# Kernel optimization log

Hardware: AMD Instinct MI355X
Metric: run time of the kernel (lower is better)

The kernel has to match this reference:

```python
import jax, jax.numpy as jnp
import numpy as np

# Module config (matches init_kwargs)
H, W = 512, 512          # in_dims
KH, KW = 32, 32          # kernel_dims
SH, SW = 16, 16          # stride
PH, PW = 8, 8            # padding
B = 64                   # batch
FULL_H, FULL_W = H + 2 * PH, W + 2 * PW            # 528, 528
NKH = 1 + (FULL_H - KH) // SH                      # 32
NKW = 1 + (FULL_W - KW) // SW                      # 32
NK = NKH * NKW                                     # 1024 output positions


def _patch_indices() -> np.ndarray:
    """Flat indices into the padded image for each sliding window.

    Reproduces the connectivity matrix columns of _create_connectivity_matrix:
    window k starts at (row*SH)*FULL_W + col*SW. Returns (NK, KH*KW) int32.
    """
    dr, dc = np.meshgrid(np.arange(KH), np.arange(KW), indexing="ij")
    off = (dr * FULL_W + dc).reshape(-1)                       # (KH*KW,)
    starts = (np.arange(NKH)[:, None] * SH * FULL_W
              + np.arange(NKW)[None, :] * SW).reshape(-1)      # (NK,)
    return (starts[:, None] + off[None, :]).astype(np.int32)


_IDX = jnp.asarray(_patch_indices())  # (NK, KH*KW), constant layout


def setup_inputs() -> dict:
    key = jax.random.key(0)
    kx, kw, kb = jax.random.split(key, 3)
    x = jax.random.normal(kx, (B, 1, H, W), dtype=jnp.float32)
    # Per-window weights = BSR values of the masked dense (padded_total, NK) matrix.
    # Xavier-normal scale of the underlying dense linear.
    std = float(np.sqrt(2.0 / (FULL_H * FULL_W + NK)))
    weight = jax.random.normal(kw, (NK, KH * KW), dtype=jnp.float32) * std
    bias = jax.random.normal(kb, (NK,), dtype=jnp.float32) * 0.01
    return {"x": x, "weight": weight, "bias": bias}


def reference(x, weight, bias):
    # x: (B, 1, H, W) -> pad -> flatten to (B, FULL_H*FULL_W)
    xp = jnp.pad(x, ((0, 0), (0, 0), (PH, PH), (PW, PW)))
    xf = xp.reshape(x.shape[0], FULL_H * FULL_W)
    # Gather the KHxKW window for every output position: (B, NK, KH*KW).
    patches = jnp.take(xf, _IDX, axis=1)
    # Untied locally-connected contraction (the block-sparse GEMM) + bias.
    out = jnp.einsum("bnk,nk->bn", patches, weight) + bias
    return out.reshape(x.shape[0], NKH, NKW)
```

## Files before the change

### kernel.cpp

```cpp
#include <hip/hip_runtime.h>

#define IMG_H 512
#define IMG_W 512
#define IMG_SZ (IMG_H * IMG_W)
#define NKH 32
#define NKW 32
#define NK 1024
#define BATCH 64
#define NTT 33
#define NTILE (NTT * NTT)
#define BG 4
#define NBLK (NTILE * BG)

typedef __attribute__((address_space(3))) char lds_char_t;
typedef const __attribute__((address_space(1))) char g_char_t;

__global__ __launch_bounds__(256)
void bslc_init(const float* __restrict__ bias, float* __restrict__ out)
{
    const int g = blockIdx.x * 256 + threadIdx.x;
    out[g] = bias[g & (NK - 1)];
}

__global__ __launch_bounds__(256, 8)
void bslc_main(const float* __restrict__ x,
               const float* __restrict__ w,
               float* __restrict__ out)
{
    __shared__ float4 xs[16 * 64];

    const int hw = blockIdx.x;
    const int xcd = hw & 7, sl = hw >> 3;
    const int q8 = NBLK >> 3, r8 = NBLK & 7;
    const int work = (xcd < r8 ? xcd * (q8 + 1)
                               : r8 * (q8 + 1) + (xcd - r8) * q8) + sl;

    const int bg  = work & 3;
    const int lin = work >> 2;
    const int tr = lin / NTT, tc = lin % NTT;

    const int t = threadIdx.x, lane = t & 63, wv = t >> 6;

    const int r0 = tr * 16 - 8, c0 = tc * 16 - 8;
    const bool interior = (tr >= 1) & (tr <= 31) & (tc >= 1) & (tc <= 31);

    if (interior) {
#pragma unroll
        for (int ii = 0; ii < 4; ++ii) {
            const int bl = 4 * ii + wv;
            const int c  = lane ^ bl;
            const int rimg = r0 + (c >> 2);
            const int cimg = c0 + (c & 3) * 4;
            const float* gp = x + (size_t)(bg * 16 + bl) * IMG_SZ
                            + (size_t)rimg * IMG_W + cimg;
            __builtin_amdgcn_global_load_lds(
                (g_char_t*)gp, (lds_char_t*)&xs[bl * 64], 16, 0, 0);
        }
    } else {
#pragma unroll
        for (int ii = 0; ii < 4; ++ii) {
            const int bl = 4 * ii + wv;
            const int c  = lane ^ bl;
            const int rimg = r0 + (c >> 2);
            const int cimg = c0 + (c & 3) * 4;
            float4 v = make_float4(0.f, 0.f, 0.f, 0.f);
            if (rimg >= 0 && rimg < IMG_H && cimg >= 0 && cimg < IMG_W)
                v = *reinterpret_cast<const float4*>(
                    x + (size_t)(bg * 16 + bl) * IMG_SZ
                      + (size_t)rimg * IMG_W + cimg);
            xs[bl * 64 + lane] = v;
        }
    }
    __syncthreads();

    const int qr = wv >> 1, qc = wv & 1;
    const int nr = tr - qr, nc = tc - qc;
    if (nr < 0 || nr >= NKH || nc < 0 || nc >= NKW) return;
    const int n = nr * NKW + nc;

    const int p  = lane >> 4;
    const int bl = lane & 15;
    const float* wq = w + (size_t)n * 1024 + (size_t)(qr * 16) * 32 + qc * 16;

    float a0 = 0.f, a1 = 0.f, a2 = 0.f, a3 = 0.f;
#pragma unroll
    for (int j = 0; j < 16; ++j) {
        const int kq = p * 16 + j;
        const float4 xv  = xs[bl * 64 + (kq ^ bl)];
        const float4 wv4 = *reinterpret_cast<const float4*>(
            wq + (kq >> 2) * 32 + (kq & 3) * 4);
        a0 = fmaf(xv.x, wv4.x, a0);
        a1 = fmaf(xv.y, wv4.y, a1);
        a2 = fmaf(xv.z, wv4.z, a2);
        a3 = fmaf(xv.w, wv4.w, a3);
    }
    float s = (a0 + a1) + (a2 + a3);
    s += __shfl_xor(s, 16, 64);
    s += __shfl_xor(s, 32, 64);
    if (p == 0)
        atomicAdd(&out[(size_t)(bg * 16 + bl) * NK + n], s);
}

extern "C" void kernel_launch(void* const* d_in, const int* in_sizes, int n_in,
                              void* d_out, int out_size, void* d_ws, size_t ws_size,
                              hipStream_t stream) {
    const float* x    = (const float*)d_in[0];
    const float* wgt  = (const float*)d_in[1];
    const float* bias = (const float*)d_in[2];
    float* out        = (float*)d_out;

    bslc_init<<<dim3(BATCH * NK / 256), 256, 0, stream>>>(bias, out);
    bslc_main<<<dim3(NBLK), 256, 0, stream>>>(x, wgt, out);
}
```

Baseline: 112.5 us.

## Restructure locally-connected kernel into per-image-row waves with register-resident weights

Each wave now owns one image row and eight batch images. It keeps the weight slices for the two overlapping output rows in registers and streams row segments straight from global memory. This removes the LDS tile staging and barrier, and the weights are reused across eight images instead of being reloaded per tile. In exchange, lanes combine partial sums with cross-lane shuffles, and the kernel issues many more atomicAdds per output, since every image row contributes its own partial sum, raising atomic contention on the output.

```diff
diff --git a/kernel.cpp b/kernel.cpp
--- a/kernel.cpp
+++ b/kernel.cpp
@@ -3,17 +3,9 @@
 #define IMG_H 512
 #define IMG_W 512
 #define IMG_SZ (IMG_H * IMG_W)
-#define NKH 32
-#define NKW 32
 #define NK 1024
-#define BATCH 64
-#define NTT 33
-#define NTILE (NTT * NTT)
-#define BG 4
-#define NBLK (NTILE * BG)
-
-typedef __attribute__((address_space(3))) char lds_char_t;
-typedef const __attribute__((address_space(1))) char g_char_t;
+#define NWAVE 4096
+#define NBLK (NWAVE / 4)
 
 __global__ __launch_bounds__(256)
 void bslc_init(const float* __restrict__ bias, float* __restrict__ out)
@@ -22,83 +14,103 @@
     out[g] = bias[g & (NK - 1)];
 }
 
-__global__ __launch_bounds__(256, 8)
+__global__ __launch_bounds__(256)
 void bslc_main(const float* __restrict__ x,
                const float* __restrict__ w,
                float* __restrict__ out)
 {
-    __shared__ float4 xs[16 * 64];
+    const int bid  = blockIdx.x;
+    const int work = (bid & 7) * (NBLK / 8) + (bid >> 3);
+    const int gw   = work * 4 + (threadIdx.x >> 6);
+    const int lane = threadIdx.x & 63;
 
-    const int hw = blockIdx.x;
-    const int xcd = hw & 7, sl = hw >> 3;
-    const int q8 = NBLK >> 3, r8 = NBLK & 7;
-    const int work = (xcd < r8 ? xcd * (q8 + 1)
-                               : r8 * (q8 + 1) + (xcd - r8) * q8) + sl;
+    const int r  = gw >> 3;
+    const int b0 = (gw & 7) * 8;
 
-    const int bg  = work & 3;
-    const int lin = work >> 2;
-    const int tr = lin / NTT, tc = lin % NTT;
+    const int cpr = r + 8;
+    const int nrh = cpr >> 4, krh = cpr & 15;
+    const int nrl = nrh - 1,  krl = krh + 16;
+    const bool vh = (nrh < 32);
+    const bool vl = (nrl >= 0);
 
-    const int t = threadIdx.x, lane = t & 63, wv = t >> 6;
+    const int  m    = (lane + 1) >> 1;
+    const int  kc0  = (lane & 1) ? 0 : 8;
+    const bool vhc  = (m < 32);
+    const bool vlc  = (m >= 1);
 
-    const int r0 = tr * 16 - 8, c0 = tc * 16 - 8;
-    const bool interior = (tr >= 1) & (tr <= 31) & (tc >= 1) & (tc <= 31);
+    const float4 z4 = make_float4(0.f, 0.f, 0.f, 0.f);
+    float4 whh[2] = {z4, z4}, whl[2] = {z4, z4};
+    float4 wlh[2] = {z4, z4}, wll[2] = {z4, z4};
 
-    if (interior) {
-#pragma unroll
-        for (int ii = 0; ii < 4; ++ii) {
-            const int bl = 4 * ii + wv;
-            const int c  = lane ^ bl;
-            const int rimg = r0 + (c >> 2);
-            const int cimg = c0 + (c & 3) * 4;
-            const float* gp = x + (size_t)(bg * 16 + bl) * IMG_SZ
-                            + (size_t)rimg * IMG_W + cimg;
-            __builtin_amdgcn_global_load_lds(
-                (g_char_t*)gp, (lds_char_t*)&xs[bl * 64], 16, 0, 0);
+    if (vh) {
+        if (vhc) {
+            const float* p = w + (size_t)(nrh * 32 + m) * 1024 + krh * 32 + kc0;
+            whh[0] = *(const float4*)p;  whh[1] = *(const float4*)(p + 4);
         }
-    } else {
-#pragma unroll
-        for (int ii = 0; ii < 4; ++ii) {
-            const int bl = 4 * ii + wv;
-            const int c  = lane ^ bl;
-            const int rimg = r0 + (c >> 2);
-            const int cimg = c0 + (c & 3) * 4;
-            float4 v = make_float4(0.f, 0.f, 0.f, 0.f);
-            if (rimg >= 0 && rimg < IMG_H && cimg >= 0 && cimg < IMG_W)
-                v = *reinterpret_cast<const float4*>(
-                    x + (size_t)(bg * 16 + bl) * IMG_SZ
-                      + (size_t)rimg * IMG_W + cimg);
-            xs[bl * 64 + lane] = v;
+        if (vlc) {
+            const float* p = w + (size_t)(nrh * 32 + m - 1) * 1024 + krh * 32 + kc0 + 16;
+            whl[0] = *(const float4*)p;  whl[1] = *(const float4*)(p + 4);
         }
     }
-    __syncthreads();
+    if (vl) {
+        if (vhc) {
+            const float* p = w + (size_t)(nrl * 32 + m) * 1024 + krl * 32 + kc0;
+            wlh[0] = *(const float4*)p;  wlh[1] = *(const float4*)(p + 4);
+        }
+        if (vlc) {
+            const float* p = w + (size_t)(nrl * 32 + m - 1) * 1024 + krl * 32 + kc0 + 16;
+            wll[0] = *(const float4*)p;  wll[1] = *(const float4*)(p + 4);
+        }
+    }
 
-    const int qr = wv >> 1, qc = wv & 1;
-    const int nr = tr - qr, nc = tc - qc;
-    if (nr < 0 || nr >= NKH || nc < 0 || nc >= NKW) return;
-    const int n = nr * NKW + nc;
+    const float* xr = x + (size_t)r * IMG_W + lane * 8;
 
-    const int p  = lane >> 4;
-    const int bl = lane & 15;
-    const float* wq = w + (size_t)n * 1024 + (size_t)(qr * 16) * 32 + qc * 16;
+#define ACC4(xv, wv, a)                                                  \
+    { a = fmaf((xv).x, (wv).x, a); a = fmaf((xv).y, (wv).y, a);          \
+      a = fmaf((xv).z, (wv).z, a); a = fmaf((xv).w, (wv).w, a); }
 
-    float a0 = 0.f, a1 = 0.f, a2 = 0.f, a3 = 0.f;
-#pragma unroll
-    for (int j = 0; j < 16; ++j) {
-        const int kq = p * 16 + j;
-        const float4 xv  = xs[bl * 64 + (kq ^ bl)];
-        const float4 wv4 = *reinterpret_cast<const float4*>(
-            wq + (kq >> 2) * 32 + (kq & 3) * 4);
-        a0 = fmaf(xv.x, wv4.x, a0);
-        a1 = fmaf(xv.y, wv4.y, a1);
-        a2 = fmaf(xv.z, wv4.z, a2);
-        a3 = fmaf(xv.w, wv4.w, a3);
+#pragma unroll 2
+    for (int bb = 0; bb < 8; ++bb) {
+        const int b = b0 + bb;
+        const float* xp = xr + (size_t)b * IMG_SZ;
+        const float4 x0 = *(const float4*)xp;
+        const float4 x1 = *(const float4*)(xp + 4);
+
+        float ahh = 0.f, ahl = 0.f, alh = 0.f, alo = 0.f;
+        ACC4(x0, whh[0], ahh); ACC4(x1, whh[1], ahh);
+        ACC4(x0, whl[0], ahl); ACC4(x1, whl[1], ahl);
+        ACC4(x0, wlh[0], alh); ACC4(x1, wlh[1], alh);
+        ACC4(x0, wll[0], alo); ACC4(x1, wll[1], alo);
+
+        {
+            const bool act = (lane == 0) || ((lane & 1) && lane <= 61);
+            if (vh) {
+                float hiN = __shfl_down(ahh, 1, 64);
+                float loN = __shfl_down(ahl, 1, 64);
+                float hi2 = ahh + ((lane == 63) ? 0.f : hiN);
+                float lo2 = ahl + ((lane == 63) ? 0.f : loN);
+                float lo21 = __shfl_down(lo2, 1, 64);
+                float lo22 = __shfl_down(lo2, 2, 64);
+                float s  = (lane == 0) ? (ahh + lo21) : (hi2 + lo22);
+                int   nc = (lane == 0) ? 0 : ((lane + 1) >> 1);
+                if (act)
+                    atomicAdd(&out[(size_t)b * NK + nrh * 32 + nc], s);
+            }
+            if (vl) {
+                float hiN = __shfl_down(alh, 1, 64);
+                float loN = __shfl_down(alo, 1, 64);
+                float hi2 = alh + ((lane == 63) ? 0.f : hiN);
+                float lo2 = alo + ((lane == 63) ? 0.f : loN);
+                float lo21 = __shfl_down(lo2, 1, 64);
+                float lo22 = __shfl_down(lo2, 2, 64);
+                float s  = (lane == 0) ? (alh + lo21) : (hi2 + lo22);
+                int   nc = (lane == 0) ? 0 : ((lane + 1) >> 1);
+                if (act)
+                    atomicAdd(&out[(size_t)b * NK + nrl * 32 + nc], s);
+            }
+        }
     }
-    float s = (a0 + a1) + (a2 + a3);
-    s += __shfl_xor(s, 16, 64);
-    s += __shfl_xor(s, 32, 64);
-    if (p == 0)
-        atomicAdd(&out[(size_t)(bg * 16 + bl) * NK + n], s);
+#undef ACC4
 }
 
 extern "C" void kernel_launch(void* const* d_in, const int* in_sizes, int n_in,
@@ -109,6 +121,6 @@
     const float* bias = (const float*)d_in[2];
     float* out        = (float*)d_out;
 
-    bslc_init<<<dim3(BATCH * NK / 256), 256, 0, stream>>>(bias, out);
+    bslc_init<<<dim3(64 * NK / 256), 256, 0, stream>>>(bias, out);
     bslc_main<<<dim3(NBLK), 256, 0, stream>>>(x, wgt, out);
 }
```

Measured after the change: 107.8 us. 4.1% less time.
